# Kernel tuning notes

Hardware: AMD Instinct MI355X
Metric: run time of the kernel (lower is better)

## Reference

```python
import jax, jax.numpy as jnp
import numpy as np

DIM = 768
HEADS = 12
SCALE = DIM ** (-0.5)  # NOTE: original scales by full dim, not per-head dim


def setup_inputs() -> dict:
    key = jax.random.key(0)
    k1, k2, k3 = jax.random.split(key, 3)
    b, n = 4, 2048
    x = jax.random.normal(k1, (b, n, DIM), dtype=jnp.float32)
    # torch Linear layout: weight [out_features, in_features]
    w_qkv = jax.random.normal(k2, (3 * DIM, DIM), dtype=jnp.float32) * (DIM ** -0.5)
    b_qkv = jnp.zeros((3 * DIM,), dtype=jnp.float32)
    w_out = jax.random.normal(k3, (DIM, DIM), dtype=jnp.float32) * (DIM ** -0.5)
    b_out = jnp.zeros((DIM,), dtype=jnp.float32)
    return {"x": x, "w_qkv": w_qkv, "b_qkv": b_qkv, "w_out": w_out, "b_out": b_out}


def reference(x, w_qkv, b_qkv, w_out, b_out):
    b, n, dim = x.shape
    h = HEADS
    d = dim // h
    qkv = x @ w_qkv.T + b_qkv                       # [b, n, 3*dim]
    # rearrange 'b n (qkv h d) -> qkv b h n d'
    qkv = qkv.reshape(b, n, 3, h, d).transpose(2, 0, 3, 1, 4)
    q, k, v = qkv[0], qkv[1], qkv[2]                # each [b, h, n, d]
    dots = jnp.einsum('bhid,bhjd->bhij', q, k) * SCALE
    attn = jax.nn.softmax(dots, axis=-1)
    out = jnp.einsum('bhij,bhjd->bhid', attn, v)    # [b, h, n, d]
    out = out.transpose(0, 2, 1, 3).reshape(b, n, h * d)
    out = out @ w_out.T + b_out
    return out
```

## Files before the change

kernel.cpp:

```cpp
#include <hip/hip_runtime.h>
#include <hip/hip_bf16.h>
#include <stdint.h>
#include <math.h>

#define HEADS 12
#define HD 64
#define NB 4
#define NSEQ 2048
#define DIM 768
#define MROWS (NB*NSEQ)
#define QKV_OUT (3*DIM)
#define QSCALE (0.03608439182435161f * 1.4426950408889634f)

typedef __bf16 bf16;
typedef __attribute__((ext_vector_type(8))) __bf16 bf16x8;
typedef __attribute__((ext_vector_type(4))) __bf16 bf16x4;
typedef __attribute__((ext_vector_type(4))) float f32x4;
typedef __attribute__((ext_vector_type(16))) float f32x16;
typedef unsigned int uint;

typedef __attribute__((address_space(1))) void gvoid_t;
typedef __attribute__((address_space(3))) void lvoid_t;
#define GLOAD_LDS16(src, dst) \
  __builtin_amdgcn_global_load_lds((gvoid_t*)(src), (lvoid_t*)(dst), 16, 0, 0)

__device__ __forceinline__ float fast_exp2(float x) {
  float r; asm("v_exp_f32 %0, %1" : "=v"(r) : "v"(x)); return r;
}
__device__ __forceinline__ uint cvtpk_bf16(float a, float b) {
  uint r; asm("v_cvt_pk_bf16_f32 %0, %1, %2" : "=v"(r) : "v"(a), "v"(b)); return r;
}
__device__ __forceinline__ void plswap(uint &a, uint &b) {
  asm("v_permlane32_swap_b32 %0, %1" : "+v"(a), "+v"(b));
}

__global__ void k_cvt3(const float* __restrict__ x, const float* __restrict__ wqkv,
                       const float* __restrict__ wout,
                       bf16* __restrict__ xb, bf16* __restrict__ wqkvb,
                       bf16* __restrict__ woutb) {
  const int n0 = MROWS * DIM / 4, n1 = QKV_OUT * DIM / 4, n2 = DIM * DIM / 4;
  int i = blockIdx.x * blockDim.x + threadIdx.x;
  const float* src; bf16* dst;
  if (i < n0)           { src = x;    dst = xb; }
  else if (i < n0 + n1) { src = wqkv; dst = wqkvb; i -= n0; }
  else if (i < n0 + n1 + n2) { src = wout; dst = woutb; i -= n0 + n1; }
  else return;
  const f32x4 v = ((const f32x4*)src)[i];
  bf16x4 o;
#pragma unroll
  for (int j = 0; j < 4; ++j) o[j] = (bf16)v[j];
  ((bf16x4*)dst)[i] = o;
}

template<int ROWBYTES>
__device__ __forceinline__ void stage_swz(const bf16* g, int grow0, int gstride,
                                          int gcol0, char* ldsbuf) {
  constexpr int CPR = ROWBYTES / 16;
  const int t = threadIdx.x;
  const int wid = t >> 6;
#pragma unroll
  for (int call = 0; call < 2; ++call) {
    const int o = call * 4096 + t * 16;
    const int r = o / ROWBYTES;
    const int c = (o % ROWBYTES) / 16;
    const int cs = c ^ (r & (CPR - 1));
    const bf16* src = g + (long)(grow0 + r) * gstride + gcol0 + cs * 8;
    char* dst = ldsbuf + call * 4096 + wid * 1024;
    GLOAD_LDS16(src, dst);
  }
}

template<int ROWBYTES>
__device__ __forceinline__ bf16x8 frag_ld(const char* buf, int row, int chunk) {
  constexpr int CPR = ROWBYTES / 16;
  const int cs = chunk ^ (row & (CPR - 1));
  return *(const bf16x8*)(buf + row * ROWBYTES + cs * 16);
}

__device__ __forceinline__ void build_pfrags(const f32x16 &p, bf16x8 *f) {
  union { uint u[4]; bf16x8 v; } A, B;
  uint a0 = cvtpk_bf16(p[0], p[1]),  b0 = cvtpk_bf16(p[4], p[5]);   plswap(a0, b0);
  uint a1 = cvtpk_bf16(p[2], p[3]),  b1 = cvtpk_bf16(p[6], p[7]);   plswap(a1, b1);
  A.u[0] = a0; A.u[1] = a1; A.u[2] = b0; A.u[3] = b1;
  uint a2 = cvtpk_bf16(p[8], p[9]),  b2 = cvtpk_bf16(p[12], p[13]); plswap(a2, b2);
  uint a3 = cvtpk_bf16(p[10], p[11]), b3 = cvtpk_bf16(p[14], p[15]); plswap(a3, b3);
  B.u[0] = a2; B.u[1] = a3; B.u[2] = b2; B.u[3] = b3;
  f[0] = A.v; f[1] = B.v;
}

__device__ __forceinline__ void qkt_step(const char* ldsc, int rbase, int kslot,
                                         const bf16x8 bq[4], f32x16 &P0, f32x16 &P1) {
#pragma unroll
  for (int r = 0; r < 16; ++r) { P0[r] = 0.f; P1[r] = 0.f; }
  __builtin_amdgcn_s_setprio(1);
#pragma unroll
  for (int ks = 0; ks < 4; ++ks) {
    const int a = (rbase ^ (ks << 5)) + kslot * 8192;
    const bf16x8 ak0 = *(const bf16x8*)(ldsc + a);
    P0 = __builtin_amdgcn_mfma_f32_32x32x16_bf16(ak0, bq[ks], P0, 0, 0, 0);
    const bf16x8 ak1 = *(const bf16x8*)(ldsc + a + 4096);
    P1 = __builtin_amdgcn_mfma_f32_32x32x16_bf16(ak1, bq[ks], P1, 0, 0, 0);
  }
  __builtin_amdgcn_s_setprio(0);
}

__device__ __forceinline__ void smpv_step(const char* ldsc, int rbase, int vslot,
                                          f32x16 &C0, f32x16 &C1, f32x16 &ot0, f32x16 &ot1,
                                          float &l_run) {
  float rs0 = 0.f, rs1 = 0.f;
#pragma unroll
  for (int r = 0; r < 16; ++r) {
    C0[r] = fast_exp2(C0[r]); rs0 += C0[r];
    C1[r] = fast_exp2(C1[r]); rs1 += C1[r];
  }
  l_run += rs0 + rs1;
  bf16x8 pf[4];
  build_pfrags(C0, &pf[0]);
  build_pfrags(C1, &pf[2]);
  __builtin_amdgcn_s_setprio(1);
#pragma unroll
  for (int s = 0; s < 4; ++s) {
    const int a = (rbase ^ (s << 5)) + 24576 + vslot * 8192;
    const bf16x8 av0 = *(const bf16x8*)(ldsc + a);
    ot0 = __builtin_amdgcn_mfma_f32_32x32x16_bf16(av0, pf[s], ot0, 0, 0, 0);
    const bf16x8 av1 = *(const bf16x8*)(ldsc + a + 4096);
    ot1 = __builtin_amdgcn_mfma_f32_32x32x16_bf16(av1, pf[s], ot1, 0, 0, 0);
  }
  __builtin_amdgcn_s_setprio(0);
}

__device__ __forceinline__ void gemm_core(const bf16* __restrict__ A, const bf16* __restrict__ Bm,
                                          int m0, int n0, f32x4 acc[4][4], char* lds) {
  const int t = threadIdx.x;
  const int lane = t & 63, wid = t >> 6;
  const int lr = lane & 15, l4 = lane >> 4;
  const int wm = wid >> 1, wn = wid & 1;
#pragma unroll
  for (int i = 0; i < 4; ++i)
#pragma unroll
    for (int j = 0; j < 4; ++j) acc[i][j] = f32x4{0.f, 0.f, 0.f, 0.f};

  stage_swz<64>(A, m0, DIM, 0, lds);
  stage_swz<64>(Bm, n0, DIM, 0, lds + 16384);
  __syncthreads();
  int cur = 0;
  const int NT = DIM / 32;
  for (int kt = 0; kt < NT; ++kt) {
    char* Acur = lds + cur * 8192;
    char* Bcur = lds + 16384 + cur * 8192;
    if (kt + 1 < NT) {
      stage_swz<64>(A, m0, DIM, (kt + 1) * 32, lds + (cur ^ 1) * 8192);
      stage_swz<64>(Bm, n0, DIM, (kt + 1) * 32, lds + 16384 + (cur ^ 1) * 8192);
    }
    bf16x8 af[4], bfr[4];
#pragma unroll
    for (int i = 0; i < 4; ++i) af[i] = frag_ld<64>(Acur, wm * 64 + i * 16 + lr, l4);
#pragma unroll
    for (int j = 0; j < 4; ++j) bfr[j] = frag_ld<64>(Bcur, wn * 64 + j * 16 + lr, l4);
#pragma unroll
    for (int i = 0; i < 4; ++i)
#pragma unroll
      for (int j = 0; j < 4; ++j)
        acc[i][j] = __builtin_amdgcn_mfma_f32_16x16x32_bf16(af[i], bfr[j], acc[i][j], 0, 0, 0);
    __syncthreads();
    cur ^= 1;
  }
}

__global__ void __launch_bounds__(256) k_qkv_gemm(const bf16* __restrict__ xb,
                                                  const bf16* __restrict__ wb,
                                                  const float* __restrict__ bqkv,
                                                  bf16* __restrict__ qb,
                                                  bf16* __restrict__ kb,
                                                  bf16* __restrict__ vtb) {
  __shared__ alignas(128) char lds[32768];
  const int m0 = blockIdx.x * 128;
  const int n0 = blockIdx.y * 128;
  const int region = n0 / DIM;
  const int t = threadIdx.x;
  const int lane = t & 63, wid = t >> 6;
  const int lr = lane & 15, l4 = lane >> 4;
  const int wm = wid >> 1, wn = wid & 1;
  f32x4 acc[4][4];

  if (region < 2) {
    gemm_core(wb, xb, n0, m0, acc, lds);
    bf16* dst0 = (region == 0) ? qb : kb;
#pragma unroll
    for (int j = 0; j < 4; ++j) {
      const int mb = m0 + wn * 64 + j * 16 + lr;
      const int bb = mb >> 11, nn = mb & 2047;
#pragma unroll
      for (int i = 0; i < 4; ++i) {
        const int o = n0 + wm * 64 + i * 16 + l4 * 4;
        const f32x4 b4 = *(const f32x4*)(bqkv + o);
        const int oc = o - region * DIM;
        const int h = oc >> 6, d = oc & 63;
        bf16x4 pk;
#pragma unroll
        for (int r = 0; r < 4; ++r) {
          float v = acc[i][j][r] + b4[r];
          if (region == 0) v *= QSCALE;
          pk[r] = (bf16)v;
        }
        *(bf16x4*)(dst0 + ((long)((bb * HEADS + h) * NSEQ + nn)) * HD + d) = pk;
      }
    }
  } else {
    gemm_core(xb, wb, m0, n0, acc, lds);
#pragma unroll
    for (int j = 0; j < 4; ++j) {
      const int o = n0 + wn * 64 + j * 16 + lr;
      const float bias = bqkv[o];
      const int oc = o - 2 * DIM;
      const int h = oc >> 6, d = oc & 63;
#pragma unroll
      for (int i = 0; i < 4; ++i) {
        const int mb = m0 + wm * 64 + i * 16 + l4 * 4;
        const int bb = mb >> 11, nn = mb & 2047;
        bf16x4 pk;
#pragma unroll
        for (int r = 0; r < 4; ++r) pk[r] = (bf16)(acc[i][j][r] + bias);
        *(bf16x4*)(vtb + ((long)((bb * HEADS + h) * HD + d)) * NSEQ + nn) = pk;
      }
    }
  }
}

__global__ void __launch_bounds__(256) k_attn(const bf16* __restrict__ qb,
                                              const bf16* __restrict__ kb,
                                              const bf16* __restrict__ vtb,
                                              bf16* __restrict__ ob) {
  __shared__ alignas(128) char lds[49152];
  char* ldsc = lds;
  const int bh = blockIdx.x;
  const int qt = blockIdx.y;
  const int t = threadIdx.x;
  const int lane = t & 63, wid = t >> 6;
  const int l31 = lane & 31, hi = lane >> 5;
  const bf16* qg = qb + (long)bh * NSEQ * HD;
  const bf16* kg = kb + (long)bh * NSEQ * HD;
  const bf16* vg = vtb + (long)bh * HD * NSEQ;
  const int q0w = qt * 128 + wid * 32;

  bf16x8 bq[4];
#pragma unroll
  for (int ks = 0; ks < 4; ++ks)
    bq[ks] = *(const bf16x8*)(qg + (long)(q0w + l31) * HD + ks * 16 + hi * 8);

  const int rbase = l31 * 128 + (((hi ^ l31) & 7) << 4);

  const int o0 = t * 16, o1 = 4096 + t * 16;
  const int r0i = o0 >> 7, cs0 = ((o0 & 127) >> 4) ^ (r0i & 7);
  const int r1i = o1 >> 7, cs1 = ((o1 & 127) >> 4) ^ (r1i & 7);
  const bf16* ksA = kg + r0i * 64 + cs0 * 8;
  const bf16* ksB = kg + r1i * 64 + cs1 * 8;
  const bf16* vsA = vg + (long)r0i * NSEQ + cs0 * 8;
  const bf16* vsB = vg + (long)r1i * NSEQ + cs1 * 8;
  const int dofs = wid << 10;

  auto stage_k = [&](int j, int slot) {
    GLOAD_LDS16(ksA + j * 4096, ldsc + slot * 8192 + dofs);
    GLOAD_LDS16(ksB + j * 4096, ldsc + slot * 8192 + 4096 + dofs);
  };
  auto stage_v = [&](int j, int slot) {
    GLOAD_LDS16(vsA + j * 64, ldsc + 24576 + slot * 8192 + dofs);
    GLOAD_LDS16(vsB + j * 64, ldsc + 24576 + slot * 8192 + 4096 + dofs);
  };

  f32x16 ot0, ot1;
#pragma unroll
  for (int r = 0; r < 16; ++r) { ot0[r] = 0.f; ot1[r] = 0.f; }
  float l_run = 0.f;

  stage_k(0, 0);
  asm volatile("s_waitcnt vmcnt(0)" ::: "memory");
  __builtin_amdgcn_s_barrier();
  asm volatile("" ::: "memory");
  f32x16 sA0, sA1, sB0, sB1;
  qkt_step(ldsc, rbase, 0, bq, sA0, sA1);
  stage_k(1, 1); stage_v(0, 0);
  stage_k(2, 2); stage_v(1, 1);

  int s0r = 0, s1r = 1, s2r = 2;
  auto iter = [&](int tt, f32x16 &C0, f32x16 &C1, f32x16 &P0, f32x16 &P1) {
    asm volatile("s_waitcnt vmcnt(4)" ::: "memory");
    __builtin_amdgcn_s_barrier();
    asm volatile("" ::: "memory");
    stage_k(tt + 3 < 32 ? tt + 3 : 31, s0r);
    stage_v(tt + 2 < 32 ? tt + 2 : 31, s2r);
    qkt_step(ldsc, rbase, s1r, bq, P0, P1);
    smpv_step(ldsc, rbase, s0r, C0, C1, ot0, ot1, l_run);
    int tmp = s0r; s0r = s1r; s1r = s2r; s2r = tmp;
  };

  for (int tp = 0; tp < 16; ++tp) {
    iter(2 * tp, sA0, sA1, sB0, sB1);
    if (tp < 15) iter(2 * tp + 1, sB0, sB1, sA0, sA1);
  }
  asm volatile("s_waitcnt vmcnt(0)" ::: "memory");
  __builtin_amdgcn_s_barrier();
  asm volatile("" ::: "memory");
  smpv_step(ldsc, rbase, s0r, sB0, sB1, ot0, ot1, l_run);

  l_run += __shfl_xor(l_run, 32);
  const float inv = 1.f / l_run;
#pragma unroll
  for (int r = 0; r < 16; ++r) { ot0[r] *= inv; ot1[r] *= inv; }
  char* tw = lds + wid * 4352;
#pragma unroll
  for (int g = 0; g < 4; ++g) {
    uint2 w0, w1;
    w0.x = cvtpk_bf16(ot0[4 * g], ot0[4 * g + 1]);
    w0.y = cvtpk_bf16(ot0[4 * g + 2], ot0[4 * g + 3]);
    w1.x = cvtpk_bf16(ot1[4 * g], ot1[4 * g + 1]);
    w1.y = cvtpk_bf16(ot1[4 * g + 2], ot1[4 * g + 3]);
    const int d0 = 8 * g + 4 * hi;
    *(uint2*)(tw + l31 * 136 + d0 * 2) = w0;
    *(uint2*)(tw + l31 * 136 + (32 + d0) * 2) = w1;
  }
  const int b_ = bh / HEADS, h_ = bh - b_ * HEADS;
#pragma unroll
  for (int pass = 0; pass < 4; ++pass) {
    const int row = pass * 8 + (lane >> 3);
    const bf16x8 vv = *(const bf16x8*)(tw + row * 136 + (lane & 7) * 16);
    *(bf16x8*)(ob + ((long)(b_ * NSEQ + q0w + row)) * DIM + h_ * 64 + (lane & 7) * 8) = vv;
  }
}

__global__ void __launch_bounds__(256) k_out_gemm(const bf16* __restrict__ ab,
                                                  const bf16* __restrict__ wob,
                                                  const float* __restrict__ bout,
                                                  float* __restrict__ out) {
  __shared__ alignas(128) char lds[32768];
  const int m0 = blockIdx.x * 128;
  const int n0 = blockIdx.y * 128;
  f32x4 acc[4][4];
  gemm_core(wob, ab, n0, m0, acc, lds);

  const int t = threadIdx.x;
  const int lane = t & 63, wid = t >> 6;
  const int lr = lane & 15, l4 = lane >> 4;
  const int wm = wid >> 1, wn = wid & 1;
#pragma unroll
  for (int j = 0; j < 4; ++j) {
    const int mb = m0 + wn * 64 + j * 16 + lr;
#pragma unroll
    for (int i = 0; i < 4; ++i) {
      const int o = n0 + wm * 64 + i * 16 + l4 * 4;
      const f32x4 v = acc[i][j] + *(const f32x4*)(bout + o);
      *(f32x4*)(out + (long)mb * DIM + o) = v;
    }
  }
}

extern "C" void kernel_launch(void* const* d_in, const int* in_sizes, int n_in,
                              void* d_out, int out_size, void* d_ws, size_t ws_size,
                              hipStream_t stream) {
  const float* x    = (const float*)d_in[0];
  const float* wqkv = (const float*)d_in[1];
  const float* bqkv = (const float*)d_in[2];
  const float* wout = (const float*)d_in[3];
  const float* bout = (const float*)d_in[4];
  float* out = (float*)d_out;
  char* ws = (char*)d_ws;

  bf16* xb    = (bf16*)(ws);
  bf16* wqkvb = (bf16*)(ws + 12582912);
  bf16* woutb = (bf16*)(ws + 16121856);
  bf16* qb    = (bf16*)(ws + 17301504);
  bf16* kb    = (bf16*)(ws + 29884416);
  bf16* vtb   = (bf16*)(ws + 42467328);
  bf16* ab    = (bf16*)(ws + 55050240);

  const int ncvt4 = MROWS * DIM / 4 + QKV_OUT * DIM / 4 + DIM * DIM / 4;
  k_cvt3<<<(ncvt4 + 255) / 256, 256, 0, stream>>>(x, wqkv, wout, xb, wqkvb, woutb);

  k_qkv_gemm<<<dim3(MROWS / 128, QKV_OUT / 128), 256, 0, stream>>>(xb, wqkvb, bqkv, qb, kb, vtb);
  k_attn<<<dim3(NB * HEADS, NSEQ / 128), 256, 0, stream>>>(qb, kb, vtb, ab);
  k_out_gemm<<<dim3(MROWS / 128, DIM / 128), 256, 0, stream>>>(ab, woutb, bout, out);
}
```

Measured before the change: 147.8 us.

## Process 64 query rows per wave in attention to reuse K/V LDS fragments

Each wave in the attention kernel now handles two 32-row query sub-tiles, so the block shrinks to 128 threads (2 waves) while still covering 128 queries. Every K and V fragment read from LDS now feeds two MFMAs instead of one, which halves LDS read traffic per unit of math. Staging is redistributed so each thread issues four global-to-LDS loads per tile, and the wait count is raised to match. The cost is many more accumulator registers per wave (eight S tiles and four output tiles), which can lower occupancy or cause spills, and there are fewer waves per block to hide latency.

```diff
diff --git a/kernel.cpp b/kernel.cpp
--- a/kernel.cpp
+++ b/kernel.cpp
@@ -89,42 +89,55 @@
 }
 
 __device__ __forceinline__ void qkt_step(const char* ldsc, int rbase, int kslot,
-                                         const bf16x8 bq[4], f32x16 &P0, f32x16 &P1) {
-#pragma unroll
-  for (int r = 0; r < 16; ++r) { P0[r] = 0.f; P1[r] = 0.f; }
+                                         const bf16x8 bq[4][2],
+                                         f32x16 &P00, f32x16 &P01,
+                                         f32x16 &P10, f32x16 &P11) {
+#pragma unroll
+  for (int r = 0; r < 16; ++r) { P00[r] = 0.f; P01[r] = 0.f; P10[r] = 0.f; P11[r] = 0.f; }
   __builtin_amdgcn_s_setprio(1);
 #pragma unroll
   for (int ks = 0; ks < 4; ++ks) {
     const int a = (rbase ^ (ks << 5)) + kslot * 8192;
     const bf16x8 ak0 = *(const bf16x8*)(ldsc + a);
-    P0 = __builtin_amdgcn_mfma_f32_32x32x16_bf16(ak0, bq[ks], P0, 0, 0, 0);
     const bf16x8 ak1 = *(const bf16x8*)(ldsc + a + 4096);
-    P1 = __builtin_amdgcn_mfma_f32_32x32x16_bf16(ak1, bq[ks], P1, 0, 0, 0);
+    P00 = __builtin_amdgcn_mfma_f32_32x32x16_bf16(ak0, bq[ks][0], P00, 0, 0, 0);
+    P10 = __builtin_amdgcn_mfma_f32_32x32x16_bf16(ak0, bq[ks][1], P10, 0, 0, 0);
+    P01 = __builtin_amdgcn_mfma_f32_32x32x16_bf16(ak1, bq[ks][0], P01, 0, 0, 0);
+    P11 = __builtin_amdgcn_mfma_f32_32x32x16_bf16(ak1, bq[ks][1], P11, 0, 0, 0);
   }
   __builtin_amdgcn_s_setprio(0);
 }
 
 __device__ __forceinline__ void smpv_step(const char* ldsc, int rbase, int vslot,
-                                          f32x16 &C0, f32x16 &C1, f32x16 &ot0, f32x16 &ot1,
-                                          float &l_run) {
-  float rs0 = 0.f, rs1 = 0.f;
+                                          f32x16 &C00, f32x16 &C01, f32x16 &C10, f32x16 &C11,
+                                          f32x16 &ot00, f32x16 &ot01,
+                                          f32x16 &ot10, f32x16 &ot11,
+                                          float &l0, float &l1) {
+  float a0 = 0.f, a1 = 0.f, b0 = 0.f, b1 = 0.f;
 #pragma unroll
   for (int r = 0; r < 16; ++r) {
-    C0[r] = fast_exp2(C0[r]); rs0 += C0[r];
-    C1[r] = fast_exp2(C1[r]); rs1 += C1[r];
-  }
-  l_run += rs0 + rs1;
-  bf16x8 pf[4];
-  build_pfrags(C0, &pf[0]);
-  build_pfrags(C1, &pf[2]);
+    C00[r] = fast_exp2(C00[r]); a0 += C00[r];
+    C01[r] = fast_exp2(C01[r]); a1 += C01[r];
+    C10[r] = fast_exp2(C10[r]); b0 += C10[r];
+    C11[r] = fast_exp2(C11[r]); b1 += C11[r];
+  }
+  l0 += a0 + a1;
+  l1 += b0 + b1;
+  bf16x8 pf0[4], pf1[4];
+  build_pfrags(C00, &pf0[0]);
+  build_pfrags(C01, &pf0[2]);
+  build_pfrags(C10, &pf1[0]);
+  build_pfrags(C11, &pf1[2]);
   __builtin_amdgcn_s_setprio(1);
 #pragma unroll
   for (int s = 0; s < 4; ++s) {
     const int a = (rbase ^ (s << 5)) + 24576 + vslot * 8192;
     const bf16x8 av0 = *(const bf16x8*)(ldsc + a);
-    ot0 = __builtin_amdgcn_mfma_f32_32x32x16_bf16(av0, pf[s], ot0, 0, 0, 0);
     const bf16x8 av1 = *(const bf16x8*)(ldsc + a + 4096);
-    ot1 = __builtin_amdgcn_mfma_f32_32x32x16_bf16(av1, pf[s], ot1, 0, 0, 0);
+    ot00 = __builtin_amdgcn_mfma_f32_32x32x16_bf16(av0, pf0[s], ot00, 0, 0, 0);
+    ot10 = __builtin_amdgcn_mfma_f32_32x32x16_bf16(av0, pf1[s], ot10, 0, 0, 0);
+    ot01 = __builtin_amdgcn_mfma_f32_32x32x16_bf16(av1, pf0[s], ot01, 0, 0, 0);
+    ot11 = __builtin_amdgcn_mfma_f32_32x32x16_bf16(av1, pf1[s], ot11, 0, 0, 0);
   }
   __builtin_amdgcn_s_setprio(0);
 }
@@ -227,10 +240,10 @@
   }
 }
 
-__global__ void __launch_bounds__(256) k_attn(const bf16* __restrict__ qb,
-                                              const bf16* __restrict__ kb,
-                                              const bf16* __restrict__ vtb,
-                                              bf16* __restrict__ ob) {
+__global__ void __launch_bounds__(128, 2) k_attn(const bf16* __restrict__ qb,
+                                                 const bf16* __restrict__ kb,
+                                                 const bf16* __restrict__ vtb,
+                                                 bf16* __restrict__ ob) {
   __shared__ alignas(128) char lds[49152];
   char* ldsc = lds;
   const int bh = blockIdx.x;
@@ -241,87 +254,98 @@
   const bf16* qg = qb + (long)bh * NSEQ * HD;
   const bf16* kg = kb + (long)bh * NSEQ * HD;
   const bf16* vg = vtb + (long)bh * HD * NSEQ;
-  const int q0w = qt * 128 + wid * 32;
-
-  bf16x8 bq[4];
+  const int q0w = qt * 128 + wid * 64;
+
+  bf16x8 bq[4][2];
 #pragma unroll
   for (int ks = 0; ks < 4; ++ks)
-    bq[ks] = *(const bf16x8*)(qg + (long)(q0w + l31) * HD + ks * 16 + hi * 8);
+#pragma unroll
+    for (int h = 0; h < 2; ++h)
+      bq[ks][h] = *(const bf16x8*)(qg + (long)(q0w + h * 32 + l31) * HD + ks * 16 + hi * 8);
 
   const int rbase = l31 * 128 + (((hi ^ l31) & 7) << 4);
 
-  const int o0 = t * 16, o1 = 4096 + t * 16;
-  const int r0i = o0 >> 7, cs0 = ((o0 & 127) >> 4) ^ (r0i & 7);
-  const int r1i = o1 >> 7, cs1 = ((o1 & 127) >> 4) ^ (r1i & 7);
-  const bf16* ksA = kg + r0i * 64 + cs0 * 8;
-  const bf16* ksB = kg + r1i * 64 + cs1 * 8;
-  const bf16* vsA = vg + (long)r0i * NSEQ + cs0 * 8;
-  const bf16* vsB = vg + (long)r1i * NSEQ + cs1 * 8;
+  const int cs = (t & 7) ^ ((t >> 3) & 7);
+  const bf16* kbase = kg + (t >> 3) * 64 + cs * 8;
+  const bf16* vbase = vg + (long)(t >> 3) * NSEQ + cs * 8;
   const int dofs = wid << 10;
 
   auto stage_k = [&](int j, int slot) {
-    GLOAD_LDS16(ksA + j * 4096, ldsc + slot * 8192 + dofs);
-    GLOAD_LDS16(ksB + j * 4096, ldsc + slot * 8192 + 4096 + dofs);
+#pragma unroll
+    for (int c = 0; c < 4; ++c)
+      GLOAD_LDS16(kbase + j * 4096 + c * 1024, ldsc + slot * 8192 + c * 2048 + dofs);
   };
   auto stage_v = [&](int j, int slot) {
-    GLOAD_LDS16(vsA + j * 64, ldsc + 24576 + slot * 8192 + dofs);
-    GLOAD_LDS16(vsB + j * 64, ldsc + 24576 + slot * 8192 + 4096 + dofs);
+#pragma unroll
+    for (int c = 0; c < 4; ++c)
+      GLOAD_LDS16(vbase + (long)j * 64 + (long)c * 32768,
+                  ldsc + 24576 + slot * 8192 + c * 2048 + dofs);
   };
 
-  f32x16 ot0, ot1;
-#pragma unroll
-  for (int r = 0; r < 16; ++r) { ot0[r] = 0.f; ot1[r] = 0.f; }
-  float l_run = 0.f;
+  f32x16 ot00, ot01, ot10, ot11;
+#pragma unroll
+  for (int r = 0; r < 16; ++r) { ot00[r] = 0.f; ot01[r] = 0.f; ot10[r] = 0.f; ot11[r] = 0.f; }
+  float l0 = 0.f, l1 = 0.f;
 
   stage_k(0, 0);
   asm volatile("s_waitcnt vmcnt(0)" ::: "memory");
   __builtin_amdgcn_s_barrier();
   asm volatile("" ::: "memory");
-  f32x16 sA0, sA1, sB0, sB1;
-  qkt_step(ldsc, rbase, 0, bq, sA0, sA1);
+  f32x16 sA00, sA01, sA10, sA11, sB00, sB01, sB10, sB11;
+  qkt_step(ldsc, rbase, 0, bq, sA00, sA01, sA10, sA11);
   stage_k(1, 1); stage_v(0, 0);
   stage_k(2, 2); stage_v(1, 1);
 
   int s0r = 0, s1r = 1, s2r = 2;
-  auto iter = [&](int tt, f32x16 &C0, f32x16 &C1, f32x16 &P0, f32x16 &P1) {
-    asm volatile("s_waitcnt vmcnt(4)" ::: "memory");
+  auto iter = [&](int tt, f32x16 &C00, f32x16 &C01, f32x16 &C10, f32x16 &C11,
+                  f32x16 &P00, f32x16 &P01, f32x16 &P10, f32x16 &P11) {
+    asm volatile("s_waitcnt vmcnt(8)" ::: "memory");
     __builtin_amdgcn_s_barrier();
     asm volatile("" ::: "memory");
     stage_k(tt + 3 < 32 ? tt + 3 : 31, s0r);
     stage_v(tt + 2 < 32 ? tt + 2 : 31, s2r);
-    qkt_step(ldsc, rbase, s1r, bq, P0, P1);
-    smpv_step(ldsc, rbase, s0r, C0, C1, ot0, ot1, l_run);
+    qkt_step(ldsc, rbase, s1r, bq, P00, P01, P10, P11);
+    smpv_step(ldsc, rbase, s0r, C00, C01, C10, C11,
+              ot00, ot01, ot10, ot11, l0, l1);
     int tmp = s0r; s0r = s1r; s1r = s2r; s2r = tmp;
   };
 
   for (int tp = 0; tp < 16; ++tp) {
-    iter(2 * tp, sA0, sA1, sB0, sB1);
-    if (tp < 15) iter(2 * tp + 1, sB0, sB1, sA0, sA1);
+    iter(2 * tp, sA00, sA01, sA10, sA11, sB00, sB01, sB10, sB11);
+    if (tp < 15) iter(2 * tp + 1, sB00, sB01, sB10, sB11, sA00, sA01, sA10, sA11);
   }
   asm volatile("s_waitcnt vmcnt(0)" ::: "memory");
   __builtin_amdgcn_s_barrier();
   asm volatile("" ::: "memory");
-  smpv_step(ldsc, rbase, s0r, sB0, sB1, ot0, ot1, l_run);
-
-  l_run += __shfl_xor(l_run, 32);
-  const float inv = 1.f / l_run;
-#pragma unroll
-  for (int r = 0; r < 16; ++r) { ot0[r] *= inv; ot1[r] *= inv; }
-  char* tw = lds + wid * 4352;
+  smpv_step(ldsc, rbase, s0r, sB00, sB01, sB10, sB11, ot00, ot01, ot10, ot11, l0, l1);
+
+  l0 += __shfl_xor(l0, 32);
+  l1 += __shfl_xor(l1, 32);
+  const float i0 = 1.f / l0, i1 = 1.f / l1;
+#pragma unroll
+  for (int r = 0; r < 16; ++r) { ot00[r] *= i0; ot01[r] *= i0; ot10[r] *= i1; ot11[r] *= i1; }
+  char* tw = lds + wid * 8704;
 #pragma unroll
   for (int g = 0; g < 4; ++g) {
+    const int d0 = 8 * g + 4 * hi;
     uint2 w0, w1;
-    w0.x = cvtpk_bf16(ot0[4 * g], ot0[4 * g + 1]);
-    w0.y = cvtpk_bf16(ot0[4 * g + 2], ot0[4 * g + 3]);
-    w1.x = cvtpk_bf16(ot1[4 * g], ot1[4 * g + 1]);
-    w1.y = cvtpk_bf16(ot1[4 * g + 2], ot1[4 * g + 3]);
-    const int d0 = 8 * g + 4 * hi;
+    w0.x = cvtpk_bf16(ot00[4 * g], ot00[4 * g + 1]);
+    w0.y = cvtpk_bf16(ot00[4 * g + 2], ot00[4 * g + 3]);
+    w1.x = cvtpk_bf16(ot01[4 * g], ot01[4 * g + 1]);
+    w1.y = cvtpk_bf16(ot01[4 * g + 2], ot01[4 * g + 3]);
     *(uint2*)(tw + l31 * 136 + d0 * 2) = w0;
     *(uint2*)(tw + l31 * 136 + (32 + d0) * 2) = w1;
+    uint2 x0, x1;
+    x0.x = cvtpk_bf16(ot10[4 * g], ot10[4 * g + 1]);
+    x0.y = cvtpk_bf16(ot10[4 * g + 2], ot10[4 * g + 3]);
+    x1.x = cvtpk_bf16(ot11[4 * g], ot11[4 * g + 1]);
+    x1.y = cvtpk_bf16(ot11[4 * g + 2], ot11[4 * g + 3]);
+    *(uint2*)(tw + (32 + l31) * 136 + d0 * 2) = x0;
+    *(uint2*)(tw + (32 + l31) * 136 + (32 + d0) * 2) = x1;
   }
   const int b_ = bh / HEADS, h_ = bh - b_ * HEADS;
 #pragma unroll
-  for (int pass = 0; pass < 4; ++pass) {
+  for (int pass = 0; pass < 8; ++pass) {
     const int row = pass * 8 + (lane >> 3);
     const bf16x8 vv = *(const bf16x8*)(tw + row * 136 + (lane & 7) * 16);
     *(bf16x8*)(ob + ((long)(b_ * NSEQ + q0w + row)) * DIM + h_ * 64 + (lane & 7) * 8) = vv;
@@ -377,6 +401,6 @@
   k_cvt3<<<(ncvt4 + 255) / 256, 256, 0, stream>>>(x, wqkv, wout, xb, wqkvb, woutb);
 
   k_qkv_gemm<<<dim3(MROWS / 128, QKV_OUT / 128), 256, 0, stream>>>(xb, wqkvb, bqkv, qb, kb, vtb);
-  k_attn<<<dim3(NB * HEADS, NSEQ / 128), 256, 0, stream>>>(qb, kb, vtb, ab);
+  k_attn<<<dim3(NB * HEADS, NSEQ / 128), 128, 0, stream>>>(qb, kb, vtb, ab);
   k_out_gemm<<<dim3(MROWS / 128, DIM / 128), 256, 0, stream>>>(ab, woutb, bout, out);
 }
```

Measured after the change: 176.6 us. 19.5% more time.
